# Optimization experiments

Measured on AMD Instinct MI355X. Metric: run time of the kernel, lower is better.

Reference implementation:

```python
import jax, jax.numpy as jnp
import numpy as np

B, S, D = 2048, 200, 64
H1, H2 = 64, 16
EPS = 1e-9
NEG_INF = -2.0**32 + 1.0


def dice(x, alpha, mean, var):
    # Dice activation at inference: BN (no center/scale) with moving stats, then
    # p = sigmoid(x_norm); out = alpha*(1-p)*x + p*x
    xn = (x - mean) * jax.lax.rsqrt(var + EPS)
    p = jax.nn.sigmoid(xn)
    return alpha * (1.0 - p) * x + p * x


def setup_inputs() -> dict:
    key = jax.random.key(0)
    ks = jax.random.split(key, 12)
    query_emb = jax.random.normal(ks[0], (B, D), dtype=jnp.float32)
    key_emb = jax.random.normal(ks[1], (B, S, D), dtype=jnp.float32)
    seq_length = jax.random.randint(ks[2], (B, 1), 1, S + 1, dtype=jnp.int32)
    # attention MLP weights (no bias): 4*D -> H1 -> H2 -> 1
    W1 = jax.random.normal(ks[3], (4 * D, H1), dtype=jnp.float32) * 0.05
    W2 = jax.random.normal(ks[4], (H1, H2), dtype=jnp.float32) * 0.05
    W3 = jax.random.normal(ks[5], (H2, 1), dtype=jnp.float32) * 0.05
    # Dice params: alpha (trainable) + BN moving stats
    alpha1 = jax.random.normal(ks[6], (H1,), dtype=jnp.float32) * 0.1
    mean1 = jax.random.normal(ks[7], (H1,), dtype=jnp.float32) * 0.1
    var1 = jax.random.uniform(ks[8], (H1,), dtype=jnp.float32, minval=0.5, maxval=1.5)
    alpha2 = jax.random.normal(ks[9], (H2,), dtype=jnp.float32) * 0.1
    mean2 = jax.random.normal(ks[10], (H2,), dtype=jnp.float32) * 0.1
    var2 = jax.random.uniform(ks[11], (H2,), dtype=jnp.float32, minval=0.5, maxval=1.5)
    return {
        "query_emb": query_emb, "key_emb": key_emb, "seq_length": seq_length,
        "W1": W1, "alpha1": alpha1, "mean1": mean1, "var1": var1,
        "W2": W2, "alpha2": alpha2, "mean2": mean2, "var2": var2,
        "W3": W3,
    }


def reference(query_emb, key_emb, seq_length, W1, alpha1, mean1, var1,
              W2, alpha2, mean2, var2, W3):
    b, s, d = key_emb.shape
    q = jnp.broadcast_to(query_emb[:, None, :], (b, s, d))
    # (B, S, 4D) interaction features
    att = jnp.concatenate([q, key_emb, q - key_emb, q * key_emb], axis=-1)
    h = dice(att @ W1, alpha1, mean1, var1)           # (B, S, H1)
    h = dice(h @ W2, alpha2, mean2, var2)             # (B, S, H2)
    score = h @ W3                                    # (B, S, 1)
    mask = (jnp.arange(s)[None, :] < seq_length).astype(score.dtype)[..., None]
    score = score * mask + (1.0 - mask) * NEG_INF
    score = jax.nn.sigmoid(score)                     # weight_normalization=False
    return jnp.sum(score * key_emb, axis=1)           # (B, D)
```

## Files before the change

kernel.cpp:

```cpp
#include <hip/hip_runtime.h>

#define NB   2048
#define SEQ  200
#define DIM  64
#define NH1  64
#define NH2  16
#define EPSF 1e-9f
#define ROWS1 4

typedef float fvec4 __attribute__((ext_vector_type(4)));
typedef short svec8 __attribute__((ext_vector_type(8)));

__device__ __forceinline__ short f2bf(float f) {
    unsigned u = __float_as_uint(f);
    u += 0x7fffu + ((u >> 16) & 1u);
    return (short)(u >> 16);
}

__global__ __launch_bounds__(256, 2)
void din_prep_kernel(const float* __restrict__ q,
                     const float* __restrict__ W1,
                     char*  __restrict__ wsA,
                     float* __restrict__ qtermws)
{
    __shared__ float Wsub[4096];
    __shared__ float Wd[4096];
    __shared__ float Wac[4096];
    const int t = threadIdx.x;

    #pragma unroll
    for (int it = 0; it < 16; ++it) {
        const int e = it * 256 + t;
        const int d = e >> 6, h = e & 63;
        const float w1a = W1[d * 64 + h];
        const float w1b = W1[(64 + d) * 64 + h];
        const float w1c = W1[(128 + d) * 64 + h];
        const float w1dv= W1[(192 + d) * 64 + h];
        Wsub[e] = w1b - w1c;
        Wac[e]  = w1a + w1c;
        Wd[e]   = w1dv;
    }
    __syncthreads();

    const int lane = t & 63;
    const int wave = t >> 6;
    const int qd4  = lane >> 4;
    const int m    = lane & 15;

    for (int r = 0; r < ROWS1; ++r) {
        const int b = blockIdx.x * ROWS1 + r;
        const float* qrow = q + (size_t)b * DIM;

        {
            const int h = wave * 16 + m;
            float s = 0.f;
            #pragma unroll
            for (int i = 0; i < 16; ++i) {
                const int d = qd4 * 16 + i;
                s = fmaf(qrow[d], Wac[d * 64 + h], s);
            }
            s += __shfl_xor(s, 16);
            s += __shfl_xor(s, 32);
            if (qd4 == 0) qtermws[(size_t)b * 64 + h] = s;
        }

        #pragma unroll
        for (int kk = 0; kk < 2; ++kk) {
            svec8 f;
            #pragma unroll
            for (int j = 0; j < 8; ++j) {
                const int d = kk * 32 + qd4 * 8 + j;
                const int h = wave * 16 + m;
                f[j] = f2bf(Wsub[d * 64 + h] + qrow[d] * Wd[d * 64 + h]);
            }
            *(svec8*)(wsA + (size_t)b * 8192 + (((wave << 1) + kk) << 10) + lane * 16) = f;
        }
    }
}

__global__ __launch_bounds__(128, 4)
void din_main_kernel(const float* __restrict__ key,
                     const int*   __restrict__ seqlen,
                     const float* __restrict__ W2,
                     const float* __restrict__ alpha1v,
                     const float* __restrict__ mean1v,
                     const float* __restrict__ var1v,
                     const float* __restrict__ alpha2v,
                     const float* __restrict__ mean2v,
                     const float* __restrict__ var2v,
                     const float* __restrict__ W3,
                     const char*  __restrict__ wsA,
                     const float* __restrict__ qtermws,
                     float* __restrict__ out)
{
    __shared__ short h1base[2][16 * NH1];
    __shared__ float obuf[2 * 64];

    const int b    = blockIdx.x;
    const int t    = threadIdx.x;
    const int lane = t & 63;
    const int wave = __builtin_amdgcn_readfirstlane(t >> 6);
    const int qd4  = lane >> 4;
    const int m    = lane & 15;

    short* h1w = h1base[wave];

    int nseq = seqlen[b];
    nseq = nseq < SEQ ? nseq : SEQ;

    svec8 wcf[4][2];
    {
        const char* fb = wsA + (size_t)b * 8192 + (size_t)lane * 16;
        #pragma unroll
        for (int c = 0; c < 4; ++c)
            #pragma unroll
            for (int kk = 0; kk < 2; ++kk)
                wcf[c][kk] = *(const svec8*)(fb + (((c << 1) + kk) << 10));
    }
    float qtermv[4];
    #pragma unroll
    for (int c = 0; c < 4; ++c) qtermv[c] = qtermws[(size_t)b * 64 + c * 16 + m];

    svec8 w2f[2];
    #pragma unroll
    for (int kk = 0; kk < 2; ++kk) {
        svec8 f;
        #pragma unroll
        for (int j = 0; j < 8; ++j)
            f[j] = f2bf(W2[(kk * 32 + qd4 * 8 + j) * NH2 + m]);
        w2f[kk] = f;
    }

    float a1v[4], m1v[4], r1v[4];
    #pragma unroll
    for (int c = 0; c < 4; ++c) {
        a1v[c] = alpha1v[c * 16 + m];
        m1v[c] = mean1v[c * 16 + m];
        r1v[c] = rsqrtf(var1v[c * 16 + m] + EPSF);
    }
    const float a2s = alpha2v[m];
    const float m2s = mean2v[m];
    const float r2s = rsqrtf(var2v[m] + EPSF);
    const float w3s = W3[m];

    fvec4 oacc0 = {0.f,0.f,0.f,0.f}, oacc1 = {0.f,0.f,0.f,0.f};
    fvec4 oacc2 = {0.f,0.f,0.f,0.f}, oacc3 = {0.f,0.f,0.f,0.f};

    const int ntiles = (nseq + 15) >> 4;
    const float* kbase = key + (size_t)b * SEQ * DIM + qd4 * 8;

    for (int tile = wave; tile < ntiles; tile += 2) {
        int row = tile * 16 + m;
        row = row < SEQ ? row : SEQ - 1;
        const float* kp = kbase + (size_t)row * DIM;
        const fvec4 kv0 = *(const fvec4*)(kp);
        const fvec4 kv1 = *(const fvec4*)(kp + 4);
        const fvec4 kv2 = *(const fvec4*)(kp + 32);
        const fvec4 kv3 = *(const fvec4*)(kp + 36);

        svec8 af0, af1;
        #pragma unroll
        for (int j = 0; j < 4; ++j) {
            af0[j]     = f2bf(kv0[j]);
            af0[4 + j] = f2bf(kv1[j]);
            af1[j]     = f2bf(kv2[j]);
            af1[4 + j] = f2bf(kv3[j]);
        }

        #pragma unroll
        for (int c = 0; c < 4; ++c) {
            const float qt = qtermv[c];
            fvec4 acc = (fvec4){qt, qt, qt, qt};
            acc = __builtin_amdgcn_mfma_f32_16x16x32_bf16(af0, wcf[c][0], acc, 0, 0, 0);
            acc = __builtin_amdgcn_mfma_f32_16x16x32_bf16(af1, wcf[c][1], acc, 0, 0, 0);
            #pragma unroll
            for (int reg = 0; reg < 4; ++reg) {
                const float x  = acc[reg];
                const float xn = (x - m1v[c]) * r1v[c];
                const float p  = 1.f / (1.f + __expf(-xn));
                const float h1 = x * (a1v[c] + p * (1.f - a1v[c]));
                h1w[(qd4 * 4 + reg) * NH1 + c * 16 + m] = f2bf(h1);
            }
        }

        const svec8 b0 = *(const svec8*)(h1w + m * NH1 + qd4 * 8);
        const svec8 b1 = *(const svec8*)(h1w + m * NH1 + 32 + qd4 * 8);
        fvec4 acc2 = (fvec4){0.f, 0.f, 0.f, 0.f};
        acc2 = __builtin_amdgcn_mfma_f32_16x16x32_bf16(b0, w2f[0], acc2, 0, 0, 0);
        acc2 = __builtin_amdgcn_mfma_f32_16x16x32_bf16(b1, w2f[1], acc2, 0, 0, 0);

        float sreg[4];
        #pragma unroll
        for (int reg = 0; reg < 4; ++reg) {
            const float x  = acc2[reg];
            const float xn = (x - m2s) * r2s;
            const float p  = 1.f / (1.f + __expf(-xn));
            const float hd = x * (a2s + p * (1.f - a2s));
            sreg[reg] = hd * w3s;
        }
        #pragma unroll
        for (int msk = 1; msk < 16; msk <<= 1) {
            sreg[0] += __shfl_xor(sreg[0], msk);
            sreg[1] += __shfl_xor(sreg[1], msk);
            sreg[2] += __shfl_xor(sreg[2], msk);
            sreg[3] += __shfl_xor(sreg[3], msk);
        }
        const int src = (m >> 2) << 4;
        const float s0b = __shfl(sreg[0], src);
        const float s1b = __shfl(sreg[1], src);
        const float s2b = __shfl(sreg[2], src);
        const float s3b = __shfl(sreg[3], src);
        const float sa = (m & 1) ? s1b : s0b;
        const float sb = (m & 1) ? s3b : s2b;
        const float sv = (m & 2) ? sb : sa;

        const int   rg = tile * 16 + m;
        const float pw = 1.f / (1.f + __expf(-sv));
        const float w  = (rg < nseq) ? pw : 0.f;

        oacc0 += w * kv0;
        oacc1 += w * kv1;
        oacc2 += w * kv2;
        oacc3 += w * kv3;
    }

    #pragma unroll
    for (int e = 0; e < 4; ++e) {
        float v0 = oacc0[e], v1 = oacc1[e], v2 = oacc2[e], v3 = oacc3[e];
        #pragma unroll
        for (int msk = 1; msk < 16; msk <<= 1) {
            v0 += __shfl_xor(v0, msk);
            v1 += __shfl_xor(v1, msk);
            v2 += __shfl_xor(v2, msk);
            v3 += __shfl_xor(v3, msk);
        }
        oacc0[e] = v0; oacc1[e] = v1; oacc2[e] = v2; oacc3[e] = v3;
    }
    if (m == 0) {
        float* op = obuf + wave * 64 + qd4 * 8;
        *(fvec4*)(op)      = oacc0;
        *(fvec4*)(op + 4)  = oacc1;
        *(fvec4*)(op + 32) = oacc2;
        *(fvec4*)(op + 36) = oacc3;
    }
    __syncthreads();
    if (t < 64)
        out[(size_t)b * DIM + t] = obuf[t] + obuf[64 + t];
}

extern "C" void kernel_launch(void* const* d_in, const int* in_sizes, int n_in,
                              void* d_out, int out_size, void* d_ws, size_t ws_size,
                              hipStream_t stream) {
    const float* q      = (const float*)d_in[0];
    const float* key    = (const float*)d_in[1];
    const int*   seqlen = (const int*)d_in[2];
    const float* W1     = (const float*)d_in[3];
    const float* alpha1 = (const float*)d_in[4];
    const float* mean1  = (const float*)d_in[5];
    const float* var1   = (const float*)d_in[6];
    const float* W2     = (const float*)d_in[7];
    const float* alpha2 = (const float*)d_in[8];
    const float* mean2  = (const float*)d_in[9];
    const float* var2   = (const float*)d_in[10];
    const float* W3     = (const float*)d_in[11];
    float* out          = (float*)d_out;

    char*  wsA     = (char*)d_ws;
    float* qtermws = (float*)((char*)d_ws + (size_t)NB * 8192);

    din_prep_kernel<<<NB / ROWS1, 256, 0, stream>>>(q, W1, wsA, qtermws);
    din_main_kernel<<<NB, 128, 0, stream>>>(key, seqlen, W2,
                                            alpha1, mean1, var1,
                                            alpha2, mean2, var2,
                                            W3, wsA, qtermws, out);
}
```

Measured before the change: 198.1 us.

## Fuse per-query W1 folding prep kernel into main attention kernel

Removes the separate prep kernel that folded query into W1 and wrote bf16 fragments plus query terms to workspace. Each main block now reads W1 directly, builds the folded bf16 weight matrix in shared memory and computes the query term with a cross-wave reduction, then loads MFMA fragments from LDS. This drops a kernel launch and the workspace round-trip (about 16 MB written and read back). In exchange, every block re-reads the full 64 KB W1 and does the folding arithmetic redundantly, and the block needs about 8 KB more LDS, which may affect occupancy.

After: 190.1 us. 4.0% less time.

```diff
diff --git a/kernel.cpp b/kernel.cpp
--- a/kernel.cpp
+++ b/kernel.cpp
@@ -6,7 +6,6 @@
 #define NH1  64
 #define NH2  16
 #define EPSF 1e-9f
-#define ROWS1 4
 
 typedef float fvec4 __attribute__((ext_vector_type(4)));
 typedef short svec8 __attribute__((ext_vector_type(8)));
@@ -17,82 +16,23 @@
     return (short)(u >> 16);
 }
 
-__global__ __launch_bounds__(256, 2)
-void din_prep_kernel(const float* __restrict__ q,
+__global__ __launch_bounds__(128, 4)
+void din_attn_kernel(const float* __restrict__ q,
+                     const float* __restrict__ key,
+                     const int*   __restrict__ seqlen,
                      const float* __restrict__ W1,
-                     char*  __restrict__ wsA,
-                     float* __restrict__ qtermws)
-{
-    __shared__ float Wsub[4096];
-    __shared__ float Wd[4096];
-    __shared__ float Wac[4096];
-    const int t = threadIdx.x;
-
-    #pragma unroll
-    for (int it = 0; it < 16; ++it) {
-        const int e = it * 256 + t;
-        const int d = e >> 6, h = e & 63;
-        const float w1a = W1[d * 64 + h];
-        const float w1b = W1[(64 + d) * 64 + h];
-        const float w1c = W1[(128 + d) * 64 + h];
-        const float w1dv= W1[(192 + d) * 64 + h];
-        Wsub[e] = w1b - w1c;
-        Wac[e]  = w1a + w1c;
-        Wd[e]   = w1dv;
-    }
-    __syncthreads();
-
-    const int lane = t & 63;
-    const int wave = t >> 6;
-    const int qd4  = lane >> 4;
-    const int m    = lane & 15;
-
-    for (int r = 0; r < ROWS1; ++r) {
-        const int b = blockIdx.x * ROWS1 + r;
-        const float* qrow = q + (size_t)b * DIM;
-
-        {
-            const int h = wave * 16 + m;
-            float s = 0.f;
-            #pragma unroll
-            for (int i = 0; i < 16; ++i) {
-                const int d = qd4 * 16 + i;
-                s = fmaf(qrow[d], Wac[d * 64 + h], s);
-            }
-            s += __shfl_xor(s, 16);
-            s += __shfl_xor(s, 32);
-            if (qd4 == 0) qtermws[(size_t)b * 64 + h] = s;
-        }
-
-        #pragma unroll
-        for (int kk = 0; kk < 2; ++kk) {
-            svec8 f;
-            #pragma unroll
-            for (int j = 0; j < 8; ++j) {
-                const int d = kk * 32 + qd4 * 8 + j;
-                const int h = wave * 16 + m;
-                f[j] = f2bf(Wsub[d * 64 + h] + qrow[d] * Wd[d * 64 + h]);
-            }
-            *(svec8*)(wsA + (size_t)b * 8192 + (((wave << 1) + kk) << 10) + lane * 16) = f;
-        }
-    }
-}
-
-__global__ __launch_bounds__(128, 4)
-void din_main_kernel(const float* __restrict__ key,
-                     const int*   __restrict__ seqlen,
-                     const float* __restrict__ W2,
                      const float* __restrict__ alpha1v,
                      const float* __restrict__ mean1v,
                      const float* __restrict__ var1v,
+                     const float* __restrict__ W2,
                      const float* __restrict__ alpha2v,
                      const float* __restrict__ mean2v,
                      const float* __restrict__ var2v,
                      const float* __restrict__ W3,
-                     const char*  __restrict__ wsA,
-                     const float* __restrict__ qtermws,
                      float* __restrict__ out)
 {
+    __shared__ short wc_bf[DIM * NH1];
+    __shared__ float qpart[2][NH1];
     __shared__ short h1base[2][16 * NH1];
     __shared__ float obuf[2 * 64];
 
@@ -105,21 +45,44 @@
 
     short* h1w = h1base[wave];
 
+    const float* qrow = q + (size_t)b * DIM;
     int nseq = seqlen[b];
     nseq = nseq < SEQ ? nseq : SEQ;
 
+    {
+        const int h = lane;
+        float qt = 0.f;
+        #pragma unroll
+        for (int i = 0; i < 32; ++i) {
+            const int d = wave * 32 + i;
+            const float qd  = qrow[d];
+            const float w1a = W1[(d)       * NH1 + h];
+            const float w1b = W1[(64 + d)  * NH1 + h];
+            const float w1c = W1[(128 + d) * NH1 + h];
+            const float w1dd= W1[(192 + d) * NH1 + h];
+            wc_bf[d * NH1 + h] = f2bf((w1b - w1c) + qd * w1dd);
+            qt = fmaf(qd, w1a + w1c, qt);
+        }
+        qpart[wave][h] = qt;
+    }
+    __syncthreads();
+
+    float qtermv[4];
+    #pragma unroll
+    for (int c = 0; c < 4; ++c)
+        qtermv[c] = qpart[0][c * 16 + m] + qpart[1][c * 16 + m];
+
     svec8 wcf[4][2];
-    {
-        const char* fb = wsA + (size_t)b * 8192 + (size_t)lane * 16;
-        #pragma unroll
-        for (int c = 0; c < 4; ++c)
+    #pragma unroll
+    for (int c = 0; c < 4; ++c)
+        #pragma unroll
+        for (int kk = 0; kk < 2; ++kk) {
+            svec8 f;
             #pragma unroll
-            for (int kk = 0; kk < 2; ++kk)
-                wcf[c][kk] = *(const svec8*)(fb + (((c << 1) + kk) << 10));
-    }
-    float qtermv[4];
-    #pragma unroll
-    for (int c = 0; c < 4; ++c) qtermv[c] = qtermws[(size_t)b * 64 + c * 16 + m];
+            for (int j = 0; j < 8; ++j)
+                f[j] = wc_bf[(kk * 32 + qd4 * 8 + j) * NH1 + c * 16 + m];
+            wcf[c][kk] = f;
+        }
 
     svec8 w2f[2];
     #pragma unroll
@@ -265,12 +228,8 @@
     const float* W3     = (const float*)d_in[11];
     float* out          = (float*)d_out;
 
-    char*  wsA     = (char*)d_ws;
-    float* qtermws = (float*)((char*)d_ws + (size_t)NB * 8192);
-
-    din_prep_kernel<<<NB / ROWS1, 256, 0, stream>>>(q, W1, wsA, qtermws);
-    din_main_kernel<<<NB, 128, 0, stream>>>(key, seqlen, W2,
+    din_attn_kernel<<<NB, 128, 0, stream>>>(q, key, seqlen, W1,
                                             alpha1, mean1, var1,
-                                            alpha2, mean2, var2,
-                                            W3, wsA, qtermws, out);
+                                            W2, alpha2, mean2, var2,
+                                            W3, out);
 }
```
